# Kernel optimization log

Hardware: AMD Instinct MI355X
Metric: run time of the kernel (lower is better)

## Reference

```python
import jax, jax.numpy as jnp
import numpy as np

T = 16                       # sample_duration
FG_THRESH, BG_HI, BG_LO = 0.5, 0.5, 0.1
ROIS_PER_IMAGE, FG_PER_IMAGE = 128, 32   # conf.TRAIN.BATCH_SIZE, round(0.25*128)
STDS = jnp.tile(jnp.array([0.1, 0.1, 0.2, 0.2], jnp.float32), T)  # BBOX_NORMALIZE_STDS tiled; means are 0


def _tube_iou(rois, gts):
    # rois [b,M,T,4], gts [b,K,T,4] -> mean per-frame IoU over non-empty frames [b,M,K]
    r = rois[:, :, None]             # [b,M,1,T,4]
    g = gts[:, None]                 # [b,1,K,T,4]
    iw = jnp.clip(jnp.minimum(r[..., 2], g[..., 2]) - jnp.maximum(r[..., 0], g[..., 0]) + 1.0, 0.0)
    ih = jnp.clip(jnp.minimum(r[..., 3], g[..., 3]) - jnp.maximum(r[..., 1], g[..., 1]) + 1.0, 0.0)
    inter = iw * ih
    ar = (r[..., 2] - r[..., 0] + 1.0) * (r[..., 3] - r[..., 1] + 1.0)
    ag = (g[..., 2] - g[..., 0] + 1.0) * (g[..., 3] - g[..., 1] + 1.0)
    r_empty = jnp.all(r == 0.0, -1)
    g_empty = jnp.all(g == 0.0, -1)
    iou = jnp.where(r_empty | g_empty, 0.0, inter / (ar + ag - inter))
    valid = ~(r_empty & g_empty)
    return iou.sum(-1) / jnp.maximum(valid.sum(-1), 1).astype(iou.dtype)


def _bbox_transform(ex, gt):
    ew = ex[..., 2] - ex[..., 0] + 1.0
    eh = ex[..., 3] - ex[..., 1] + 1.0
    ecx = ex[..., 0] + 0.5 * ew
    ecy = ex[..., 1] + 0.5 * eh
    gw = gt[..., 2] - gt[..., 0] + 1.0
    gh = gt[..., 3] - gt[..., 1] + 1.0
    gcx = gt[..., 0] + 0.5 * gw
    gcy = gt[..., 1] + 0.5 * gh
    return jnp.stack([(gcx - ecx) / ew, (gcy - ecy) / eh,
                      jnp.log(gw / ew), jnp.log(gh / eh)], axis=-1)


def _sample_one(ov, lab, key):
    # ov, lab: [M]; jit-safe fg/bg sampling matching the torch control flow
    M = ov.shape[0]
    k1, k2, k3, k4 = jax.random.split(key, 4)
    fg = ov >= FG_THRESH
    bg = (ov < BG_HI) & (ov >= BG_LO)
    fg_num = fg.sum()
    bg_num = bg.sum()
    # random permutation with fg (resp. bg) indices first
    order_fg = jnp.argsort(jnp.where(fg, jax.random.uniform(k1, (M,)), 2.0))
    order_bg = jnp.argsort(jnp.where(bg, jax.random.uniform(k2, (M,)), 2.0))
    fg_this = jnp.where(bg_num > 0, jnp.minimum(FG_PER_IMAGE, fg_num),
                        jnp.where(fg_num > 0, ROIS_PER_IMAGE, 0))
    r = jnp.arange(ROIS_PER_IMAGE)
    fg_repl = order_fg[(jax.random.uniform(k3, (ROIS_PER_IMAGE,)) * jnp.maximum(fg_num, 1)).astype(jnp.int32)]
    fg_idx = jnp.where(bg_num > 0, order_fg[r], fg_repl)  # no-replacement when bg exists, else with replacement
    bg_idx = order_bg[(jax.random.uniform(k4, (ROIS_PER_IMAGE,)) * jnp.maximum(bg_num, 1)).astype(jnp.int32)]
    is_fg = r < fg_this
    keep = jnp.where(is_fg, fg_idx, bg_idx)
    return keep, jnp.where(is_fg, lab[keep], 0.0)


def _forward(all_tubes, gt_boxes, gt_tubes_all):
    b, N, _ = all_tubes.shape
    A = gt_boxes.shape[1]
    # gt tube coords + label of first nonzero-labelled frame
    gt_tubes = gt_boxes[..., :4].reshape(b, A, T * 4)
    fr_lab = gt_boxes[..., 4]                                    # [b,A,T]
    has = jnp.any(fr_lab != 0, axis=2)
    first = jnp.argmax(fr_lab != 0, axis=2)
    labels_gt = jnp.where(has, jnp.take_along_axis(fr_lab, first[..., None], 2)[..., 0], 0.0)
    # scatter tube coords into frames [round(start), round(end)] (vectorized mask-scatter)
    sf = jnp.round(all_tubes[..., 3]).astype(jnp.int32)[..., None]
    ef = jnp.round(all_tubes[..., 6]).astype(jnp.int32)[..., None]
    f = jnp.arange(T)[None, None]
    fmask = ((f >= sf) & (f <= ef)).astype(all_tubes.dtype)      # [b,N,T]
    coords = all_tubes[..., jnp.array([1, 2, 4, 5])]             # [b,N,4]
    all_rois = fmask[..., None] * coords[:, :, None, :]          # [b,N,T,4]
    off = jnp.broadcast_to(jnp.arange(b, dtype=all_rois.dtype)[:, None, None], (b, N, 1))
    all_rois = jnp.concatenate([off, all_rois.reshape(b, N, T * 4)], axis=2)
    # append gt boxes/tubes as extra proposals (batch col = 0)
    gt_app = jnp.concatenate([jnp.zeros((b, A, 1), all_rois.dtype), gt_tubes], axis=2)
    all_rois = jnp.concatenate([all_rois, gt_app], axis=1)       # [b,N+A,1+4T]
    gt_tubes_app = jnp.concatenate([jnp.zeros((b, A, 1), all_tubes.dtype), gt_tubes_all[..., :-1]], axis=2)
    all_tubes_c = jnp.concatenate([all_tubes, gt_tubes_app], axis=1)  # [b,N+A,7]
    # IoU overlaps + gt assignment
    ov = _tube_iou(all_rois[..., 1:].reshape(b, N + A, T, 4),
                   gt_tubes.reshape(b, A, T, 4))                 # [b,N+A,A]
    max_ov = ov.max(axis=2)
    gt_asg = ov.argmax(axis=2)
    labels = jnp.take_along_axis(labels_gt, gt_asg, axis=1)      # [b,N+A]
    # fg/bg sampling (fixed key -> deterministic)
    keys = jax.random.split(jax.random.key(42), b)
    keep, labels_b = jax.vmap(_sample_one)(max_ov, labels, keys)  # [b,R]
    rois_b = jnp.take_along_axis(all_rois, keep[..., None], axis=1)
    rois_b = rois_b.at[..., 0].set(jnp.arange(b, dtype=rois_b.dtype)[:, None])
    tubes_b = jnp.take_along_axis(all_tubes_c, keep[..., None], axis=1)
    tubes_b = tubes_b.at[..., 0].set(jnp.arange(b, dtype=tubes_b.dtype)[:, None])
    asg_k = jnp.take_along_axis(gt_asg, keep, axis=1)
    gt_rois_b = jnp.take_along_axis(gt_tubes, asg_k[..., None], axis=1)  # [b,R,4T]
    tgt = _bbox_transform(rois_b[..., 1:].reshape(b, ROIS_PER_IMAGE, T, 4),
                          gt_rois_b.reshape(b, ROIS_PER_IMAGE, T, 4)).reshape(b, ROIS_PER_IMAGE, T * 4)
    tgt = tgt / STDS
    pos = (labels_b > 0)[..., None]
    bbox_targets = jnp.where(pos, tgt, 0.0)
    inside = jnp.where(pos, jnp.ones_like(tgt), 0.0)
    outside = (inside > 0).astype(tgt.dtype)
    return rois_b, tubes_b, labels_b, bbox_targets, inside, outside


def setup_inputs() -> dict:
    key = jax.random.key(0)
    ks = jax.random.split(key, 9)
    b, N, A = 8, 20000, 5
    x1 = jax.random.uniform(ks[0], (b, N), minval=0.0, maxval=200.0)
    y1 = jax.random.uniform(ks[1], (b, N), minval=0.0, maxval=200.0)
    x2 = x1 + jax.random.uniform(ks[2], (b, N), minval=8.0, maxval=120.0)
    y2 = y1 + jax.random.uniform(ks[3], (b, N), minval=8.0, maxval=120.0)
    sf = jax.random.randint(ks[4], (b, N), 0, T).astype(jnp.float32)
    ef = jnp.minimum(sf + jax.random.randint(ks[5], (b, N), 0, T).astype(jnp.float32), T - 1.0)
    bidx = jnp.broadcast_to(jnp.arange(b, dtype=jnp.float32)[:, None], (b, N))
    all_tubes = jnp.stack([bidx, x1, y1, sf, x2, y2, ef], axis=-1)
    gx1 = jax.random.uniform(ks[6], (b, A, T), minval=0.0, maxval=200.0)
    gy1 = jax.random.uniform(ks[7], (b, A, T), minval=0.0, maxval=200.0)
    gx2 = gx1 + 60.0
    gy2 = gy1 + 60.0
    glab = jax.random.randint(ks[8], (b, A), 1, 21).astype(jnp.float32)[..., None]
    gt_boxes = jnp.stack([gx1, gy1, gx2, gy2, jnp.broadcast_to(glab, (b, A, T))], axis=-1)
    gt_tubes_all = jnp.concatenate([
        jnp.zeros((b, A, 1)), gx1.min(-1, keepdims=True), gy1.min(-1, keepdims=True),
        jnp.zeros((b, A, 1)), gx2.max(-1, keepdims=True), gy2.max(-1, keepdims=True),
        jnp.full((b, A, 1), T - 1.0)], axis=-1).astype(jnp.float32)
    return {"all_tubes": all_tubes, "gt_boxes": gt_boxes, "gt_tubes_all": gt_tubes_all}


def reference(all_tubes, gt_boxes, gt_tubes_all):
    return _forward(all_tubes, gt_boxes, gt_tubes_all)
```

## Files before the change

### kernel.cpp

```cpp
#include <hip/hip_runtime.h>
#include <stdint.h>

#define T 16
#define NB 8
#define NROI 20000
#define NA 5
#define MM (NROI + NA)
#define MMPAD 20224
#define RPI 128
#define FGPI 32
#define NBLK 79
#define NBLK2 20
#define SORTCAP 32768
#define LCAP 16384

__host__ __device__ __forceinline__ void tf2x32(uint32_t k0, uint32_t k1,
                                                uint32_t x0, uint32_t x1,
                                                uint32_t& o0, uint32_t& o1) {
  uint32_t ks2 = k0 ^ k1 ^ 0x1BD11BDAu;
  x0 += k0; x1 += k1;
#define ROUND(r) { x0 += x1; x1 = (x1 << (r)) | (x1 >> (32 - (r))); x1 ^= x0; }
  ROUND(13) ROUND(15) ROUND(26) ROUND(6)
  x0 += k1; x1 += ks2 + 1u;
  ROUND(17) ROUND(29) ROUND(16) ROUND(24)
  x0 += ks2; x1 += k0 + 2u;
  ROUND(13) ROUND(15) ROUND(26) ROUND(6)
  x0 += k0; x1 += k1 + 3u;
  ROUND(17) ROUND(29) ROUND(16) ROUND(24)
  x0 += k1; x1 += ks2 + 4u;
  ROUND(13) ROUND(15) ROUND(26) ROUND(6)
  x0 += ks2; x1 += k0 + 5u;
#undef ROUND
  o0 = x0; o1 = x1;
}

__device__ __forceinline__ uint32_t rbits32(uint32_t k0, uint32_t k1, uint32_t i) {
  uint32_t a, b; tf2x32(k0, k1, 0u, i, a, b); return a ^ b;
}
__device__ __forceinline__ float uni01(uint32_t bits) {
  return __uint_as_float((bits >> 9) | 0x3f800000u) - 1.0f;
}

struct Keys { uint32_t k[NB][4][2]; };

__global__ __launch_bounds__(256) void k_iou(const float* __restrict__ tubes,
                                             const float* __restrict__ gtb,
                                             unsigned long long* __restrict__ pk) {
  int img = blockIdx.y;
  int a = blockIdx.z;
  int b = blockIdx.x;
  int tid = threadIdx.x;
  int n = b * 256 + tid;
  bool valid = n < MM;
  int nn = valid ? n : MM - 1;
  bool isroi = nn < NROI;

  __shared__ float tub[256 * 7];
  __shared__ float4 g4[NA][T];
  __shared__ float gar[NA][T];
  {
    int rcnt = min(256, NROI - b * 256);
    int f4cnt = (rcnt * 7) >> 2;
    const float4* src = (const float4*)(tubes + (size_t)img * NROI * 7 + (size_t)b * 256 * 7);
    float4* dst = (float4*)tub;
    for (int i = tid; i < f4cnt; i += 256) dst[i] = src[i];
  }
  for (int i = tid; i < NA * T; i += 256) {
    int aa = i / T, t = i - aa * T;
    const float* p = gtb + (((size_t)img * NA + aa) * T + t) * 5;
    float4 v = make_float4(p[0], p[1], p[2], p[3]);
    g4[aa][t] = v;
    gar[aa][t] = (v.z - v.x + 1.0f) * (v.w - v.y + 1.0f);
  }
  __syncthreads();

  float s = 0.0f;
  if (isroi) {
    const float* p = &tub[tid * 7];
    float rx1 = p[1], ry1 = p[2], rx2 = p[4], ry2 = p[5];
    int sf = (int)rintf(p[3]), ef = (int)rintf(p[6]);
    float rar = (rx2 - rx1 + 1.0f) * (ry2 - ry1 + 1.0f);
#pragma unroll
    for (int t = 0; t < T; ++t) {
      float4 gg = g4[a][t]; float ag = gar[a][t];
      float iw = fmaxf(fminf(rx2, gg.z) - fmaxf(rx1, gg.x) + 1.0f, 0.0f);
      float ih = fmaxf(fminf(ry2, gg.w) - fmaxf(ry1, gg.y) + 1.0f, 0.0f);
      float inter = iw * ih;
      float q = inter / (rar + ag - inter);
      s += ((t >= sf) && (t <= ef)) ? q : 0.0f;
    }
  } else {
    int ga = nn - NROI;
#pragma unroll
    for (int t = 0; t < T; ++t) {
      float4 e = g4[ga][t]; float ar = gar[ga][t];
      float4 gg = g4[a][t]; float ag = gar[a][t];
      float iw = fmaxf(fminf(e.z, gg.z) - fmaxf(e.x, gg.x) + 1.0f, 0.0f);
      float ih = fmaxf(fminf(e.w, gg.w) - fmaxf(e.y, gg.y) + 1.0f, 0.0f);
      float inter = iw * ih;
      s += inter / (ar + ag - inter);
    }
  }
  if (valid) {
    float ovv = s / 16.0f;
    unsigned long long pkv = ((unsigned long long)__float_as_uint(ovv) << 3)
                           | (unsigned long long)(7 - a);
    atomicMax(&pk[(size_t)img * MMPAD + n], pkv);
  }
}

__global__ __launch_bounds__(1024) void k_classify(const unsigned long long* __restrict__ pk,
                                                   uint64_t* __restrict__ slots,
                                                   int* __restrict__ cnts2,
                                                   int* __restrict__ mins2,
                                                   Keys keys) {
  int img = blockIdx.y;
  int b = blockIdx.x;
  int tid = threadIdx.x;
  int n = b * 1024 + tid;
  bool valid = n < MM;
  int nn = valid ? n : MM - 1;
  int lane = tid & 63;
  int w = tid >> 6;

  unsigned long long p = pk[(size_t)img * MMPAD + nn];
  float best = __uint_as_float((uint32_t)(p >> 3));

  bool isfg = valid && (best >= 0.5f);
  bool isbg = valid && (best < 0.5f) && (best >= 0.1f);

  __shared__ int wcnt[16][2];
  __shared__ int wmn[16][2];
  unsigned long long mfg = __ballot(isfg);
  unsigned long long mbg = __ballot(isbg);
  unsigned long long mnf = __ballot(valid && !isfg);
  unsigned long long mnb = __ballot(valid && !isbg);
  int wavebase = b * 1024 + w * 64;
  if (lane == 0) {
    wcnt[w][0] = __popcll(mfg);
    wcnt[w][1] = __popcll(mbg);
    wmn[w][0] = mnf ? (wavebase + __ffsll(mnf) - 1) : 0x7FFFFFFF;
    wmn[w][1] = mnb ? (wavebase + __ffsll(mnb) - 1) : 0x7FFFFFFF;
  }
  __syncthreads();

  if (tid == 0) {
    int tf = 0, tb = 0, mf = 0x7FFFFFFF, mb = 0x7FFFFFFF;
#pragma unroll
    for (int w2 = 0; w2 < 16; ++w2) {
      tf += wcnt[w2][0]; tb += wcnt[w2][1];
      mf = min(mf, wmn[w2][0]); mb = min(mb, wmn[w2][1]);
    }
    int idx = img * NBLK2 + b;
    cnts2[idx]                = tf;
    cnts2[NB * NBLK2 + idx]   = tb;
    mins2[idx]                = mf;
    mins2[NB * NBLK2 + idx]   = mb;
  }

  int pf = 0, pb = 0;
  for (int w2 = 0; w2 < w; ++w2) { pf += wcnt[w2][0]; pb += wcnt[w2][1]; }
  unsigned long long below = (1ULL << lane) - 1ULL;
  uint64_t* slotF = slots + (size_t)(img * 2 + 0) * SORTCAP + b * 1024;
  uint64_t* slotB = slots + (size_t)(img * 2 + 1) * SORTCAP + b * 1024;
  if (isfg) {
    int pos = pf + __popcll(mfg & below);
    uint32_t m = rbits32(keys.k[img][0][0], keys.k[img][0][1], (uint32_t)n) >> 9;
    slotF[pos] = ((uint64_t)m << 32) | (uint32_t)n;
  }
  if (isbg) {
    int pos = pb + __popcll(mbg & below);
    uint32_t m = rbits32(keys.k[img][1][0], keys.k[img][1][1], (uint32_t)n) >> 9;
    slotB[pos] = ((uint64_t)m << 32) | (uint32_t)n;
  }
}

__global__ __launch_bounds__(1024) void k_sortsample(const float* __restrict__ tubes,
                                                     const float* __restrict__ gtb,
                                                     const float* __restrict__ gta,
                                                     const unsigned long long* __restrict__ pk,
                                                     uint64_t* __restrict__ slots,
                                                     const int* __restrict__ cnts2,
                                                     const int* __restrict__ mins2,
                                                     Keys keys,
                                                     float* __restrict__ out) {
  __shared__ uint64_t buf[LCAP];
  __shared__ int scnt[NBLK2], spref[NBLK2 + 1];
  __shared__ int s_tot, s_oth, s_mn;
  __shared__ int s_keep[RPI];
  __shared__ int s_ak[RPI];
  __shared__ float s_lab[RPI];
  __shared__ unsigned char s_own[RPI];

  int list = blockIdx.x;
  int img = list >> 1;
  int which = list & 1;
  int tid = threadIdx.x;
  uint64_t* arr = slots + (size_t)(img * 2 + which) * SORTCAP;
  const int* cn = cnts2 + which * NB * NBLK2 + img * NBLK2;
  const int* co = cnts2 + (1 - which) * NB * NBLK2 + img * NBLK2;
  const int* mn = mins2 + which * NB * NBLK2 + img * NBLK2;

  if (tid < NBLK2) scnt[tid] = cn[tid];
  __syncthreads();
  if (tid == 0) {
    int acc = 0, mmn = 0x7FFFFFFF, oth = 0;
#pragma unroll
    for (int bb = 0; bb < NBLK2; ++bb) {
      spref[bb] = acc; acc += scnt[bb];
      mmn = min(mmn, mn[bb]); oth += co[bb];
    }
    spref[NBLK2] = acc; s_tot = acc; s_mn = mmn; s_oth = oth;
  }
  __syncthreads();
  int cnt = s_tot, min_non = s_mn;
  int fg_num = (which == 0) ? cnt : s_oth;
  int bg_num = (which == 0) ? s_oth : cnt;

  int n2 = 2; while (n2 < cnt) n2 <<= 1;
  bool ldsPath = (n2 <= LCAP);

  if (cnt > 0 && ldsPath) {
    for (int s = tid; s < NBLK2 * 1024; s += 1024) {
      int bb = s >> 10, i = s & 1023;
      if (i < scnt[bb]) buf[spref[bb] + i] = arr[s];
    }
    for (int i = cnt + tid; i < n2; i += 1024) buf[i] = ~0ULL;
    __syncthreads();
    if (cnt > 1) {
      for (int k = 2; k <= n2; k <<= 1) {
        for (int j = k >> 1; j; j >>= 1) {
          for (int i = tid; i < n2; i += 1024) {
            int ixj = i ^ j;
            if (ixj > i) {
              uint64_t a = buf[i], bv = buf[ixj];
              bool up = (i & k) == 0;
              if (up ? (a > bv) : (a < bv)) { buf[i] = bv; buf[ixj] = a; }
            }
          }
          __syncthreads();
        }
      }
    }
  } else if (cnt > 1) {
    for (int bb = 0; bb < NBLK2; ++bb) {
      uint64_t v = 0; int c = scnt[bb];
      if (tid < c) v = arr[bb * 1024 + tid];
      __syncthreads();
      if (tid < c) arr[spref[bb] + tid] = v;
      __syncthreads();
    }
    for (int i = cnt + tid; i < n2; i += 1024) arr[i] = ~0ULL;
    __syncthreads();
    for (int k = 2; k <= n2; k <<= 1) {
      for (int j = k >> 1; j; j >>= 1) {
        for (int i = tid; i < n2; i += 1024) {
          int ixj = i ^ j;
          if (ixj > i) {
            uint64_t a = arr[i], bv = arr[ixj];
            bool up = (i & k) == 0;
            if (up ? (a > bv) : (a < bv)) { arr[i] = bv; arr[ixj] = a; }
          }
        }
        __syncthreads();
      }
    }
  }
  __syncthreads();

  float* o_rois = out;
  float* o_tub = out + (size_t)NB * RPI * 65;
  float* o_lab = o_tub + (size_t)NB * RPI * 7;
  float* o_tgt = o_lab + (size_t)NB * RPI;
  float* o_in  = o_tgt + (size_t)NB * RPI * 64;
  float* o_ou  = o_in  + (size_t)NB * RPI * 64;

  int fg_this = (bg_num > 0) ? min(FGPI, fg_num) : (fg_num > 0 ? RPI : 0);

#define MY_AT(i) (ldsPath ? (int)(uint32_t)(buf[i] & 0xffffffffULL) : (int)(uint32_t)(arr[i] & 0xffffffffULL))

  if (tid < RPI) {
    int r = tid;
    bool is_fg = r < fg_this;
    bool own = (is_fg == (which == 0));
    s_own[r] = own ? 1 : 0;
    if (own) {
      int keep;
      if (which == 0) {
        if (bg_num > 0) {
          keep = MY_AT(r);
        } else {
          float u3 = uni01(rbits32(keys.k[img][2][0], keys.k[img][2][1], (uint32_t)r));
          int q = (int)(u3 * (float)max(fg_num, 1));
          keep = (q >= fg_num)
                   ? ((fg_num >= MM) ? MY_AT(MM - 1) : min_non)
                   : MY_AT(q);
        }
      } else {
        float u4 = uni01(rbits32(keys.k[img][3][0], keys.k[img][3][1], (uint32_t)r));
        int qb = (int)(u4 * (float)max(bg_num, 1));
        keep = (qb >= bg_num)
                 ? ((bg_num >= MM) ? MY_AT(MM - 1) : min_non)
                 : MY_AT(qb);
      }

      unsigned long long pkv = pk[(size_t)img * MMPAD + keep];
      int ak = 7 - (int)(pkv & 7ULL);
      float glab = gtb[(((size_t)img * NA + ak) * T + 0) * 5 + 4];
      float lab = is_fg ? glab : 0.0f;
      s_keep[r] = keep; s_ak[r] = ak; s_lab[r] = lab;

      size_t row = (size_t)img * RPI + r;
      float* pt = o_tub + row * 7;
      o_rois[row * 65] = (float)img;
      pt[0] = (float)img;
      if (keep < NROI) {
        const float* p = tubes + ((size_t)img * NROI + keep) * 7;
#pragma unroll
        for (int cc = 1; cc < 7; ++cc) pt[cc] = p[cc];
      } else {
        const float* p = gta + ((size_t)img * NA + (keep - NROI)) * 7;
#pragma unroll
        for (int cc = 1; cc < 7; ++cc) pt[cc] = p[cc - 1];
      }
      o_lab[row] = lab;
    }
  }
#undef MY_AT
  __syncthreads();

  for (int i = tid; i < RPI * T; i += 1024) {
    int rl = i >> 4;
    if (!s_own[rl]) continue;
    int t = i & 15;
    size_t row = (size_t)img * RPI + rl;
    int keep = s_keep[rl];
    int ak = s_ak[rl];
    float lab = s_lab[rl];
    bool pos = lab > 0.0f;
    float posf = pos ? 1.0f : 0.0f;

    float ex1, ey1, ex2, ey2;
    if (keep < NROI) {
      const float* p = tubes + ((size_t)img * NROI + keep) * 7;
      int sf = (int)rintf(p[3]), ef = (int)rintf(p[6]);
      bool in = (t >= sf) && (t <= ef);
      ex1 = in ? p[1] : 0.0f; ey1 = in ? p[2] : 0.0f;
      ex2 = in ? p[4] : 0.0f; ey2 = in ? p[5] : 0.0f;
    } else {
      const float* p = gtb + (((size_t)img * NA + (keep - NROI)) * T + t) * 5;
      ex1 = p[0]; ey1 = p[1]; ex2 = p[2]; ey2 = p[3];
    }

    float* pr = o_rois + row * 65 + 1 + 4 * t;
    pr[0] = ex1; pr[1] = ey1; pr[2] = ex2; pr[3] = ey2;

    const float* gp = gtb + (((size_t)img * NA + ak) * T + t) * 5;
    float gx1 = gp[0], gy1 = gp[1], gx2 = gp[2], gy2 = gp[3];
    float ew = ex2 - ex1 + 1.0f, eh = ey2 - ey1 + 1.0f;
    float ecx = ex1 + 0.5f * ew, ecy = ey1 + 0.5f * eh;
    float gw = gx2 - gx1 + 1.0f, gh = gy2 - gy1 + 1.0f;
    float gcx = gx1 + 0.5f * gw, gcy = gy1 + 0.5f * gh;
    float t0 = ((gcx - ecx) / ew) / 0.1f;
    float t1 = ((gcy - ecy) / eh) / 0.1f;
    float t2 = logf(gw / ew) / 0.2f;
    float t3 = logf(gh / eh) / 0.2f;

    *(float4*)(o_tgt + row * 64 + 4 * t) =
        make_float4(pos ? t0 : 0.0f, pos ? t1 : 0.0f, pos ? t2 : 0.0f, pos ? t3 : 0.0f);
    float4 pf4 = make_float4(posf, posf, posf, posf);
    *(float4*)(o_in + row * 64 + 4 * t) = pf4;
    *(float4*)(o_ou + row * 64 + 4 * t) = pf4;
  }
}

extern "C" void kernel_launch(void* const* d_in, const int* in_sizes, int n_in,
                              void* d_out, int out_size, void* d_ws, size_t ws_size,
                              hipStream_t stream) {
  const float* tubes = (const float*)d_in[0];
  const float* gtb   = (const float*)d_in[1];
  const float* gta   = (const float*)d_in[2];
  float* out = (float*)d_out;
  char* ws = (char*)d_ws;

  Keys keys;
  for (int img = 0; img < NB; ++img) {
    uint32_t r0, r1; tf2x32(0u, 42u, 0u, (uint32_t)img, r0, r1);
    for (int j = 0; j < 4; ++j) {
      uint32_t a, b; tf2x32(r0, r1, 0u, (uint32_t)j, a, b);
      keys.k[img][j][0] = a; keys.k[img][j][1] = b;
    }
  }

  int* cnts2 = (int*)ws;
  int* mins2 = (int*)(ws + 1280);
  unsigned long long* pk = (unsigned long long*)(ws + 4096);
  uint64_t* slots = (uint64_t*)(ws + 1298432);

  hipMemsetAsync(pk, 0, (size_t)NB * MMPAD * 8, stream);
  dim3 gI(NBLK, NB, NA);
  k_iou<<<gI, 256, 0, stream>>>(tubes, gtb, pk);
  dim3 gC(NBLK2, NB);
  k_classify<<<gC, 1024, 0, stream>>>(pk, slots, cnts2, mins2, keys);
  k_sortsample<<<16, 1024, 0, stream>>>(tubes, gtb, gta, pk, slots, cnts2, mins2, keys, out);
}
```

Measured before the change: 48.35 us.

## Replace LDS bitonic sort with histogram bucketing plus per-query rank selection

The full bitonic sort of up to 16K keys in LDS is replaced by a 2048-bucket histogram on the top key bits, a wave-shuffle prefix scan, and an atomic scatter into buckets. Each of the 128 sampled positions then binary-searches its bucket and finds the element of the requested rank by brute-force counting within that bucket. This removes the many sort passes and barriers, but the result depends on buckets staying small, and scatter order inside buckets is nondeterministic.

Measured after the change: 43.15 us. 1.12x faster.

```diff
diff --git a/kernel.cpp b/kernel.cpp
--- a/kernel.cpp
+++ b/kernel.cpp
@@ -13,6 +13,7 @@
 #define NBLK2 20
 #define SORTCAP 32768
 #define LCAP 16384
+#define NBUCK 2048
 
 __host__ __device__ __forceinline__ void tf2x32(uint32_t k0, uint32_t k1,
                                                 uint32_t x0, uint32_t x1,
@@ -185,6 +186,9 @@
                                                      Keys keys,
                                                      float* __restrict__ out) {
   __shared__ uint64_t buf[LCAP];
+  __shared__ int hist[NBUCK];
+  __shared__ int pref[NBUCK + 1];
+  __shared__ int wsum[16];
   __shared__ int scnt[NBLK2], spref[NBLK2 + 1];
   __shared__ int s_tot, s_oth, s_mn;
   __shared__ int s_keep[RPI];
@@ -196,12 +200,14 @@
   int img = list >> 1;
   int which = list & 1;
   int tid = threadIdx.x;
+  int lane = tid & 63, wv = tid >> 6;
   uint64_t* arr = slots + (size_t)(img * 2 + which) * SORTCAP;
   const int* cn = cnts2 + which * NB * NBLK2 + img * NBLK2;
   const int* co = cnts2 + (1 - which) * NB * NBLK2 + img * NBLK2;
   const int* mn = mins2 + which * NB * NBLK2 + img * NBLK2;
 
   if (tid < NBLK2) scnt[tid] = cn[tid];
+  for (int i = tid; i < NBUCK; i += 1024) hist[i] = 0;
   __syncthreads();
   if (tid == 0) {
     int acc = 0, mmn = 0x7FFFFFFF, oth = 0;
@@ -216,32 +222,49 @@
   int cnt = s_tot, min_non = s_mn;
   int fg_num = (which == 0) ? cnt : s_oth;
   int bg_num = (which == 0) ? s_oth : cnt;
-
-  int n2 = 2; while (n2 < cnt) n2 <<= 1;
-  bool ldsPath = (n2 <= LCAP);
+  bool ldsPath = (cnt <= LCAP);
 
   if (cnt > 0 && ldsPath) {
     for (int s = tid; s < NBLK2 * 1024; s += 1024) {
       int bb = s >> 10, i = s & 1023;
-      if (i < scnt[bb]) buf[spref[bb] + i] = arr[s];
-    }
-    for (int i = cnt + tid; i < n2; i += 1024) buf[i] = ~0ULL;
+      if (i < scnt[bb]) {
+        uint64_t key = arr[s];
+        atomicAdd(&hist[(int)(key >> 44)], 1);
+      }
+    }
     __syncthreads();
-    if (cnt > 1) {
-      for (int k = 2; k <= n2; k <<= 1) {
-        for (int j = k >> 1; j; j >>= 1) {
-          for (int i = tid; i < n2; i += 1024) {
-            int ixj = i ^ j;
-            if (ixj > i) {
-              uint64_t a = buf[i], bv = buf[ixj];
-              bool up = (i & k) == 0;
-              if (up ? (a > bv) : (a < bv)) { buf[i] = bv; buf[ixj] = a; }
-            }
-          }
-          __syncthreads();
-        }
-      }
-    }
+    {
+      int a0 = hist[2 * tid], a1 = hist[2 * tid + 1];
+      int ps = a0 + a1;
+      int v = ps;
+      for (int off = 1; off < 64; off <<= 1) {
+        int u = __shfl_up(v, off);
+        if (lane >= off) v += u;
+      }
+      if (lane == 63) wsum[wv] = v;
+      __syncthreads();
+      if (tid == 0) {
+        int acc = 0;
+        for (int i = 0; i < 16; ++i) { int x = wsum[i]; wsum[i] = acc; acc += x; }
+        pref[NBUCK] = acc;
+      }
+      __syncthreads();
+      int excl = v - ps + wsum[wv];
+      pref[2 * tid] = excl;
+      pref[2 * tid + 1] = excl + a0;
+      hist[2 * tid] = excl;
+      hist[2 * tid + 1] = excl + a0;
+    }
+    __syncthreads();
+    for (int s = tid; s < NBLK2 * 1024; s += 1024) {
+      int bb = s >> 10, i = s & 1023;
+      if (i < scnt[bb]) {
+        uint64_t key = arr[s];
+        int pos = atomicAdd(&hist[(int)(key >> 44)], 1);
+        buf[pos] = key;
+      }
+    }
+    __syncthreads();
   } else if (cnt > 1) {
     for (int bb = 0; bb < NBLK2; ++bb) {
       uint64_t v = 0; int c = scnt[bb];
@@ -250,6 +273,7 @@
       if (tid < c) arr[spref[bb] + tid] = v;
       __syncthreads();
     }
+    int n2 = 2; while (n2 < cnt) n2 <<= 1;
     for (int i = cnt + tid; i < n2; i += 1024) arr[i] = ~0ULL;
     __syncthreads();
     for (int k = 2; k <= n2; k <<= 1) {
@@ -265,8 +289,8 @@
         __syncthreads();
       }
     }
-  }
-  __syncthreads();
+    __syncthreads();
+  }
 
   float* o_rois = out;
   float* o_tub = out + (size_t)NB * RPI * 65;
@@ -277,7 +301,28 @@
 
   int fg_this = (bg_num > 0) ? min(FGPI, fg_num) : (fg_num > 0 ? RPI : 0);
 
-#define MY_AT(i) (ldsPath ? (int)(uint32_t)(buf[i] & 0xffffffffULL) : (int)(uint32_t)(arr[i] & 0xffffffffULL))
+#define RANKQ(L, OUTV) {                                               \
+    int l_ = (L);                                                      \
+    if (ldsPath) {                                                     \
+      int lo_ = 0, hi_ = NBUCK;                                        \
+      while (hi_ - lo_ > 1) {                                          \
+        int mid_ = (lo_ + hi_) >> 1;                                   \
+        if (pref[mid_] <= l_) lo_ = mid_; else hi_ = mid_;             \
+      }                                                                \
+      int base_ = pref[lo_], cnt_ = pref[lo_ + 1] - base_;             \
+      int ll_ = l_ - base_;                                            \
+      uint64_t ans_ = 0;                                               \
+      for (int i_ = 0; i_ < cnt_; ++i_) {                              \
+        uint64_t ki_ = buf[base_ + i_];                                \
+        int cl_ = 0;                                                   \
+        for (int j_ = 0; j_ < cnt_; ++j_) cl_ += (buf[base_ + j_] < ki_); \
+        if (cl_ == ll_) { ans_ = ki_; break; }                         \
+      }                                                                \
+      OUTV = (int)(uint32_t)(ans_ & 0xffffffffULL);                    \
+    } else {                                                           \
+      OUTV = (int)(uint32_t)(arr[l_] & 0xffffffffULL);                 \
+    }                                                                  \
+  }
 
   if (tid < RPI) {
     int r = tid;
@@ -288,20 +333,24 @@
       int keep;
       if (which == 0) {
         if (bg_num > 0) {
-          keep = MY_AT(r);
+          RANKQ(r, keep)
         } else {
           float u3 = uni01(rbits32(keys.k[img][2][0], keys.k[img][2][1], (uint32_t)r));
           int q = (int)(u3 * (float)max(fg_num, 1));
-          keep = (q >= fg_num)
-                   ? ((fg_num >= MM) ? MY_AT(MM - 1) : min_non)
-                   : MY_AT(q);
+          if (q >= fg_num) {
+            if (fg_num >= MM) { RANKQ(MM - 1, keep) } else keep = min_non;
+          } else {
+            RANKQ(q, keep)
+          }
         }
       } else {
         float u4 = uni01(rbits32(keys.k[img][3][0], keys.k[img][3][1], (uint32_t)r));
         int qb = (int)(u4 * (float)max(bg_num, 1));
-        keep = (qb >= bg_num)
-                 ? ((bg_num >= MM) ? MY_AT(MM - 1) : min_non)
-                 : MY_AT(qb);
+        if (qb >= bg_num) {
+          if (bg_num >= MM) { RANKQ(MM - 1, keep) } else keep = min_non;
+        } else {
+          RANKQ(qb, keep)
+        }
       }
 
       unsigned long long pkv = pk[(size_t)img * MMPAD + keep];
@@ -326,7 +375,7 @@
       o_lab[row] = lab;
     }
   }
-#undef MY_AT
+#undef RANKQ
   __syncthreads();
 
   for (int i = tid; i < RPI * T; i += 1024) {
```
